# Optimization experiments

Hardware: AMD Instinct MI355X
Metric: run time of the kernel (lower is better)

Reference implementation:

```python
import jax, jax.numpy as jnp
import numpy as np

DIM = 512
NUM_HEADS = 8
HEAD_DIM = DIM // NUM_HEADS
SCALE = HEAD_DIM ** -0.5
B, N = 8, 1024


def setup_inputs() -> dict:
    key = jax.random.key(0)
    k1, k2, k3, k4, k5 = jax.random.split(key, 5)
    x = jax.random.normal(k1, (B, N, DIM), dtype=jnp.float32)
    rpe_bias = jax.random.normal(k2, (1, NUM_HEADS, N, N), dtype=jnp.float32)
    # torch Linear weights: [out_features, in_features], y = x @ W.T
    qkv_w = jax.random.normal(k3, (3 * DIM, DIM), dtype=jnp.float32) * (DIM ** -0.5)
    proj_w = jax.random.normal(k4, (DIM, DIM), dtype=jnp.float32) * (DIM ** -0.5)
    proj_b = jax.random.normal(k5, (DIM,), dtype=jnp.float32) * 0.01
    return {"x": x, "rpe_bias": rpe_bias, "qkv_w": qkv_w, "proj_w": proj_w, "proj_b": proj_b}


def reference(x, rpe_bias, qkv_w, proj_w, proj_b):
    b, n, c = x.shape
    h, d = NUM_HEADS, HEAD_DIM
    # qkv projection (no bias): [B,N,3C] -> [3,B,H,N,D]
    qkv = (x @ qkv_w.T).reshape(b, n, 3, h, d).transpose(2, 0, 3, 1, 4)
    q, k, v = qkv[0], qkv[1], qkv[2]
    attn = jnp.einsum('bhnd,bhmd->bhnm', q, k) * SCALE + rpe_bias
    attn = jax.nn.softmax(attn, axis=-1)  # dropout p=0 -> identity
    out = jnp.einsum('bhnm,bhmd->bhnd', attn, v)
    out = out.transpose(0, 2, 1, 3).reshape(b, n, c)
    return out @ proj_w.T + proj_b
```

## Files before the change

### kernel.cpp

```cpp
#include <hip/hip_runtime.h>
#include <hip/hip_bf16.h>

#define B_    8
#define N_    1024
#define DIM_  512
#define H_    8
#define DH_   64
#define SCALE_ 0.125f

typedef unsigned short u16;
typedef __attribute__((ext_vector_type(8))) short bf16x8;
typedef __attribute__((ext_vector_type(4))) float f32x4;

__device__ __forceinline__ u16 f2bf(float f) {
  union { float f; unsigned u; } v; v.f = f;
  return (u16)((v.u + 0x7fffu + ((v.u >> 16) & 1u)) >> 16);
}
__device__ __forceinline__ unsigned pack2(float a, float b) {
  return (unsigned)f2bf(a) | ((unsigned)f2bf(b) << 16);
}
__device__ __forceinline__ void cp16(const void* g, void* l) {
  __builtin_amdgcn_global_load_lds(
      (const __attribute__((address_space(1))) unsigned*)g,
      (__attribute__((address_space(3))) unsigned*)l, 16, 0, 0);
}

__global__ __launch_bounds__(256) void convert_kernel(
    const float* __restrict__ X, const float* __restrict__ Wq,
    const float* __restrict__ Wp, u16* __restrict__ Xb,
    u16* __restrict__ Wqb, u16* __restrict__ Wpb) {
  const int NX4 = (B_ * N_ * DIM_) / 4;
  const int NQ4 = (3 * DIM_ * DIM_) / 4;
  const int NP4 = (DIM_ * DIM_) / 4;
  const int total = NX4 + NQ4 + NP4;
  const int stride = gridDim.x * 256;
  for (int i = blockIdx.x * 256 + threadIdx.x; i < total; i += stride) {
    const float* s; u16* d; int off;
    if (i < NX4)            { s = X;  d = Xb;  off = i; }
    else if (i < NX4 + NQ4) { s = Wq; d = Wqb; off = i - NX4; }
    else                    { s = Wp; d = Wpb; off = i - NX4 - NQ4; }
    float4 f = *(const float4*)(s + (size_t)off * 4);
    uint2 u; u.x = pack2(f.x, f.y); u.y = pack2(f.z, f.w);
    *(uint2*)(d + (size_t)off * 4) = u;
  }
}

__global__ __launch_bounds__(256) void qkv_gemm(
    const u16* __restrict__ Ab, const u16* __restrict__ Bb,
    u16* __restrict__ Q, u16* __restrict__ K, u16* __restrict__ Vt) {
  __shared__ __align__(16) u16 sA[128 * 64];
  __shared__ __align__(16) u16 sB[128 * 64];
  const int t = threadIdx.x;
  const int wv = t >> 6, lane = t & 63, quad = (lane >> 4) & 3, l15 = lane & 15;
  const int wr = wv >> 1, wc = wv & 1;
  const int m0 = blockIdx.y * 128;
  const int n0 = blockIdx.x * 128;

  const int srow = lane >> 3;
  const int schunk = (lane & 7) ^ srow;
  const size_t ga = (size_t)(m0 + srow) * DIM_ + schunk * 8;
  const size_t gb = (size_t)(n0 + srow) * DIM_ + schunk * 8;

  f32x4 zero = {0.f, 0.f, 0.f, 0.f};
  f32x4 acc[4][4];
#pragma unroll
  for (int i = 0; i < 4; i++)
#pragma unroll
    for (int j = 0; j < 4; j++) acc[i][j] = zero;

  for (int k0 = 0; k0 < DIM_; k0 += 64) {
    __syncthreads();
#pragma unroll
    for (int i = 0; i < 4; i++) {
      const int rb = 32 * wv + 8 * i;
      cp16(Ab + ga + (size_t)rb * DIM_ + k0, &sA[rb * 64]);
      cp16(Bb + gb + (size_t)rb * DIM_ + k0, &sB[rb * 64]);
    }
    __syncthreads();
#pragma unroll
    for (int ks = 0; ks < 2; ks++) {
      bf16x8 af[4], bfv[4];
#pragma unroll
      for (int i = 0; i < 4; i++)
        af[i] = *(const bf16x8*)&sA[(wr * 64 + 16 * i + l15) * 64 +
                                    (((ks << 2) | quad) ^ (l15 & 7)) * 8];
#pragma unroll
      for (int j = 0; j < 4; j++)
        bfv[j] = *(const bf16x8*)&sB[(wc * 64 + 16 * j + l15) * 64 +
                                     (((ks << 2) | quad) ^ (l15 & 7)) * 8];
#pragma unroll
      for (int i = 0; i < 4; i++)
#pragma unroll
        for (int j = 0; j < 4; j++)
          acc[i][j] = __builtin_amdgcn_mfma_f32_16x16x32_bf16(af[i], bfv[j], acc[i][j], 0, 0, 0);
    }
  }

  const int tsel = n0 >> 9;
#pragma unroll
  for (int j = 0; j < 4; j++) {
    const int jg = n0 + wc * 64 + 16 * j + l15;
    const int h = (jg >> 6) & 7, d = jg & 63;
#pragma unroll
    for (int i = 0; i < 4; i++) {
      const int mbase = m0 + wr * 64 + 16 * i + quad * 4;
      const int b = mbase >> 10, nb = mbase & 1023;
      const size_t bh = (size_t)(b * H_ + h);
      if (tsel == 2) {
        ushort4 v4;
        v4.x = f2bf(acc[i][j][0]); v4.y = f2bf(acc[i][j][1]);
        v4.z = f2bf(acc[i][j][2]); v4.w = f2bf(acc[i][j][3]);
        *(ushort4*)&Vt[(bh * DH_ + d) * N_ + nb] = v4;
      } else {
        u16* dst = (tsel == 0 ? Q : K);
#pragma unroll
        for (int rr = 0; rr < 4; rr++)
          dst[(bh * N_ + nb + rr) * DH_ + d] = f2bf(acc[i][j][rr]);
      }
    }
  }
}

__global__ __launch_bounds__(256) void attn_kernel(
    const u16* __restrict__ Q, const u16* __restrict__ K,
    const u16* __restrict__ Vt, const float* __restrict__ bias,
    u16* __restrict__ AO) {
  __shared__ __align__(16) u16 sK[64 * 72];
  __shared__ __align__(16) u16 sV[64 * 72];
  __shared__ __align__(16) u16 sP[64 * 72];
  const int t = threadIdx.x;
  const int wv = t >> 6, lane = t & 63, quad = (lane >> 4) & 3, l15 = lane & 15;
  const int n0 = blockIdx.x * 64;
  const int bh = blockIdx.y;
  const int b = bh >> 3, h = bh & 7;
  const int r = t >> 2, c = (t & 3) << 4;

  const int qg = n0 + 16 * wv + l15;
  bf16x8 qf0, qf1;
  {
    const u16* qsrc = Q + (((size_t)bh << 10) + qg) * DH_ + (quad << 3);
    qf0 = *(const bf16x8*)qsrc;
    qf1 = *(const bf16x8*)(qsrc + 32);
  }

  const float* bp = bias + (((size_t)h << 10) + qg) * N_ + (quad << 2);
  const u16* kbase = K + (((size_t)bh << 10) + r) * DH_ + c;
  const u16* vbase = Vt + (((size_t)bh << 6) + r) * N_ + c;

  f32x4 zero = {0.f, 0.f, 0.f, 0.f};
  f32x4 O[4];
  O[0] = zero; O[1] = zero; O[2] = zero; O[3] = zero;
  float lsum = 0.f;

  uint4 ka = *(const uint4*)kbase, kb2 = *(const uint4*)(kbase + 8);
  uint4 va = *(const uint4*)vbase, vb2 = *(const uint4*)(vbase + 8);
  float4 bias4[4];
#pragma unroll
  for (int cb = 0; cb < 4; cb++) bias4[cb] = *(const float4*)(bp + 16 * cb);

  for (int kt = 0; kt < 16; kt++) {
    __syncthreads();
    *(uint4*)&sK[r * 72 + c] = ka;  *(uint4*)&sK[r * 72 + c + 8] = kb2;
    *(uint4*)&sV[r * 72 + c] = va;  *(uint4*)&sV[r * 72 + c + 8] = vb2;
    if (kt < 15) {
      const u16* kn = kbase + (size_t)(kt + 1) * 64 * DH_;
      const u16* vn = vbase + (kt + 1) * 64;
      ka = *(const uint4*)kn; kb2 = *(const uint4*)(kn + 8);
      va = *(const uint4*)vn; vb2 = *(const uint4*)(vn + 8);
    }
    __syncthreads();

    f32x4 S[4];
    S[0] = zero; S[1] = zero; S[2] = zero; S[3] = zero;
#pragma unroll
    for (int ks = 0; ks < 2; ks++) {
      const bf16x8 qf = ks ? qf1 : qf0;
#pragma unroll
      for (int cb = 0; cb < 4; cb++) {
        bf16x8 kf = *(const bf16x8*)&sK[(16 * cb + l15) * 72 + ks * 32 + (quad << 3)];
        S[cb] = __builtin_amdgcn_mfma_f32_16x16x32_bf16(kf, qf, S[cb], 0, 0, 0);
      }
    }

#pragma unroll
    for (int cb = 0; cb < 4; cb++) {
      float p0 = __expf(fmaf(S[cb][0], SCALE_, bias4[cb].x));
      float p1 = __expf(fmaf(S[cb][1], SCALE_, bias4[cb].y));
      float p2 = __expf(fmaf(S[cb][2], SCALE_, bias4[cb].z));
      float p3 = __expf(fmaf(S[cb][3], SCALE_, bias4[cb].w));
      lsum += (p0 + p1) + (p2 + p3);
      uint2 pk;
      pk.x = pack2(p0, p1);
      pk.y = pack2(p2, p3);
      *(uint2*)&sP[(16 * wv + l15) * 72 + 16 * cb + (quad << 2)] = pk;
    }
    if (kt < 15) {
      const float* bn = bp + (kt + 1) * 64;
#pragma unroll
      for (int cb = 0; cb < 4; cb++) bias4[cb] = *(const float4*)(bn + 16 * cb);
    }
    asm volatile("s_waitcnt lgkmcnt(0)" ::: "memory");

#pragma unroll
    for (int ks = 0; ks < 2; ks++) {
      bf16x8 pf = *(const bf16x8*)&sP[(16 * wv + l15) * 72 + ks * 32 + (quad << 3)];
#pragma unroll
      for (int cb = 0; cb < 4; cb++) {
        bf16x8 vf = *(const bf16x8*)&sV[(16 * cb + l15) * 72 + ks * 32 + (quad << 3)];
        O[cb] = __builtin_amdgcn_mfma_f32_16x16x32_bf16(vf, pf, O[cb], 0, 0, 0);
      }
    }
  }

  lsum += __shfl_xor(lsum, 16);
  lsum += __shfl_xor(lsum, 32);
  const float inv = 1.f / lsum;
#pragma unroll
  for (int cb = 0; cb < 4; cb++) {
    ushort4 o4;
    o4.x = f2bf(O[cb][0] * inv); o4.y = f2bf(O[cb][1] * inv);
    o4.z = f2bf(O[cb][2] * inv); o4.w = f2bf(O[cb][3] * inv);
    *(ushort4*)&AO[(((size_t)b << 10) + qg) * DIM_ + h * DH_ + 16 * cb + (quad << 2)] = o4;
  }
}

__global__ __launch_bounds__(256) void proj_gemm(
    const u16* __restrict__ Ab, const u16* __restrict__ Bb,
    const float* __restrict__ Pb, float* __restrict__ Out) {
  __shared__ __align__(16) u16 sA[128 * 64];
  __shared__ __align__(16) u16 sB[128 * 64];
  const int t = threadIdx.x;
  const int wv = t >> 6, lane = t & 63, quad = (lane >> 4) & 3, l15 = lane & 15;
  const int wr = wv >> 1, wc = wv & 1;
  const int m0 = blockIdx.y * 128;
  const int n0 = blockIdx.x * 128;

  const int srow = lane >> 3;
  const int schunk = (lane & 7) ^ srow;
  const size_t ga = (size_t)(m0 + srow) * DIM_ + schunk * 8;
  const size_t gb = (size_t)(n0 + srow) * DIM_ + schunk * 8;

  f32x4 zero = {0.f, 0.f, 0.f, 0.f};
  f32x4 acc[4][4];
#pragma unroll
  for (int i = 0; i < 4; i++)
#pragma unroll
    for (int j = 0; j < 4; j++) acc[i][j] = zero;

  for (int k0 = 0; k0 < DIM_; k0 += 64) {
    __syncthreads();
#pragma unroll
    for (int i = 0; i < 4; i++) {
      const int rb = 32 * wv + 8 * i;
      cp16(Ab + ga + (size_t)rb * DIM_ + k0, &sA[rb * 64]);
      cp16(Bb + gb + (size_t)rb * DIM_ + k0, &sB[rb * 64]);
    }
    __syncthreads();
#pragma unroll
    for (int ks = 0; ks < 2; ks++) {
      bf16x8 af[4], bfv[4];
#pragma unroll
      for (int i = 0; i < 4; i++)
        af[i] = *(const bf16x8*)&sA[(wr * 64 + 16 * i + l15) * 64 +
                                    (((ks << 2) | quad) ^ (l15 & 7)) * 8];
#pragma unroll
      for (int j = 0; j < 4; j++)
        bfv[j] = *(const bf16x8*)&sB[(wc * 64 + 16 * j + l15) * 64 +
                                     (((ks << 2) | quad) ^ (l15 & 7)) * 8];
#pragma unroll
      for (int i = 0; i < 4; i++)
#pragma unroll
        for (int j = 0; j < 4; j++)
          acc[i][j] = __builtin_amdgcn_mfma_f32_16x16x32_bf16(af[i], bfv[j], acc[i][j], 0, 0, 0);
    }
  }

#pragma unroll
  for (int j = 0; j < 4; j++) {
    const int jg = n0 + wc * 64 + 16 * j + l15;
    const float pb = Pb[jg];
#pragma unroll
    for (int i = 0; i < 4; i++) {
      const int mbase = m0 + wr * 64 + 16 * i + quad * 4;
#pragma unroll
      for (int rr = 0; rr < 4; rr++)
        Out[(size_t)(mbase + rr) * DIM_ + jg] = acc[i][j][rr] + pb;
    }
  }
}

extern "C" void kernel_launch(void* const* d_in, const int* in_sizes, int n_in,
                              void* d_out, int out_size, void* d_ws, size_t ws_size,
                              hipStream_t stream) {
  const float* x      = (const float*)d_in[0];
  const float* rpe    = (const float*)d_in[1];
  const float* qkv_w  = (const float*)d_in[2];
  const float* proj_w = (const float*)d_in[3];
  const float* proj_b = (const float*)d_in[4];
  float* out = (float*)d_out;

  const size_t perbuf = (size_t)B_ * N_ * DIM_;
  u16* Xb  = (u16*)d_ws;
  u16* Q   = Xb + perbuf;
  u16* K   = Q + perbuf;
  u16* Vt  = K + perbuf;
  u16* Wqb = Vt + perbuf;
  u16* Wpb = Wqb + (size_t)3 * DIM_ * DIM_;
  u16* AO  = Xb;

  convert_kernel<<<2560, 256, 0, stream>>>(x, qkv_w, proj_w, Xb, Wqb, Wpb);
  qkv_gemm<<<dim3(12, 64), 256, 0, stream>>>(Xb, Wqb, Q, K, Vt);
  attn_kernel<<<dim3(16, 64), 256, 0, stream>>>(Q, K, Vt, rpe, AO);
  proj_gemm<<<dim3(4, 64), 256, 0, stream>>>(AO, Wpb, proj_b, out);
}
```

Baseline: 176.6 us.

## Shrink GEMM tiles, keep P in registers, swizzle LDS, remap attention grid

The QKV and projection GEMMs switch from 128x128 to 128x64 tiles, doubling the block count and adding launch bounds for higher occupancy. The attention kernel drops the sP shared buffer and feeds P straight from registers into 16x16x16 MFMAs. It replaces padded K/V shared layouts with XOR-swizzled ones, adds s_setprio around the MFMA phases, and remaps blocks so neighbouring blocks share a head and reuse the bias in L2. Together these cut LDS traffic and barriers, in exchange for more V fragment loads and more MFMA instructions.

After: 173.7 us. Within noise of the previous version (-1.7%).

```diff
diff --git a/kernel.cpp b/kernel.cpp
--- a/kernel.cpp
+++ b/kernel.cpp
@@ -10,6 +10,7 @@
 
 typedef unsigned short u16;
 typedef __attribute__((ext_vector_type(8))) short bf16x8;
+typedef __attribute__((ext_vector_type(4))) short bf16x4;
 typedef __attribute__((ext_vector_type(4))) float f32x4;
 
 __device__ __forceinline__ u16 f2bf(float f) {
@@ -45,16 +46,15 @@
   }
 }
 
-__global__ __launch_bounds__(256) void qkv_gemm(
+__global__ __launch_bounds__(256, 4) void qkv_gemm(
     const u16* __restrict__ Ab, const u16* __restrict__ Bb,
     u16* __restrict__ Q, u16* __restrict__ K, u16* __restrict__ Vt) {
   __shared__ __align__(16) u16 sA[128 * 64];
-  __shared__ __align__(16) u16 sB[128 * 64];
+  __shared__ __align__(16) u16 sB[64 * 64];
   const int t = threadIdx.x;
   const int wv = t >> 6, lane = t & 63, quad = (lane >> 4) & 3, l15 = lane & 15;
-  const int wr = wv >> 1, wc = wv & 1;
   const int m0 = blockIdx.y * 128;
-  const int n0 = blockIdx.x * 128;
+  const int n0 = blockIdx.x * 64;
 
   const int srow = lane >> 3;
   const int schunk = (lane & 7) ^ srow;
@@ -62,9 +62,9 @@
   const size_t gb = (size_t)(n0 + srow) * DIM_ + schunk * 8;
 
   f32x4 zero = {0.f, 0.f, 0.f, 0.f};
-  f32x4 acc[4][4];
-#pragma unroll
-  for (int i = 0; i < 4; i++)
+  f32x4 acc[2][4];
+#pragma unroll
+  for (int i = 0; i < 2; i++)
 #pragma unroll
     for (int j = 0; j < 4; j++) acc[i][j] = zero;
 
@@ -74,22 +74,26 @@
     for (int i = 0; i < 4; i++) {
       const int rb = 32 * wv + 8 * i;
       cp16(Ab + ga + (size_t)rb * DIM_ + k0, &sA[rb * 64]);
+    }
+#pragma unroll
+    for (int i = 0; i < 2; i++) {
+      const int rb = 16 * wv + 8 * i;
       cp16(Bb + gb + (size_t)rb * DIM_ + k0, &sB[rb * 64]);
     }
     __syncthreads();
 #pragma unroll
     for (int ks = 0; ks < 2; ks++) {
-      bf16x8 af[4], bfv[4];
-#pragma unroll
-      for (int i = 0; i < 4; i++)
-        af[i] = *(const bf16x8*)&sA[(wr * 64 + 16 * i + l15) * 64 +
+      bf16x8 af[2], bfv[4];
+#pragma unroll
+      for (int i = 0; i < 2; i++)
+        af[i] = *(const bf16x8*)&sA[(wv * 32 + 16 * i + l15) * 64 +
                                     (((ks << 2) | quad) ^ (l15 & 7)) * 8];
 #pragma unroll
       for (int j = 0; j < 4; j++)
-        bfv[j] = *(const bf16x8*)&sB[(wc * 64 + 16 * j + l15) * 64 +
+        bfv[j] = *(const bf16x8*)&sB[(16 * j + l15) * 64 +
                                      (((ks << 2) | quad) ^ (l15 & 7)) * 8];
 #pragma unroll
-      for (int i = 0; i < 4; i++)
+      for (int i = 0; i < 2; i++)
 #pragma unroll
         for (int j = 0; j < 4; j++)
           acc[i][j] = __builtin_amdgcn_mfma_f32_16x16x32_bf16(af[i], bfv[j], acc[i][j], 0, 0, 0);
@@ -99,11 +103,11 @@
   const int tsel = n0 >> 9;
 #pragma unroll
   for (int j = 0; j < 4; j++) {
-    const int jg = n0 + wc * 64 + 16 * j + l15;
+    const int jg = n0 + 16 * j + l15;
     const int h = (jg >> 6) & 7, d = jg & 63;
 #pragma unroll
-    for (int i = 0; i < 4; i++) {
-      const int mbase = m0 + wr * 64 + 16 * i + quad * 4;
+    for (int i = 0; i < 2; i++) {
+      const int mbase = m0 + wv * 32 + 16 * i + quad * 4;
       const int b = mbase >> 10, nb = mbase & 1023;
       const size_t bh = (size_t)(b * H_ + h);
       if (tsel == 2) {
@@ -121,95 +125,111 @@
   }
 }
 
-__global__ __launch_bounds__(256) void attn_kernel(
+__global__ __launch_bounds__(256, 4) void attn_kernel(
     const u16* __restrict__ Q, const u16* __restrict__ K,
     const u16* __restrict__ Vt, const float* __restrict__ bias,
     u16* __restrict__ AO) {
-  __shared__ __align__(16) u16 sK[64 * 72];
-  __shared__ __align__(16) u16 sV[64 * 72];
-  __shared__ __align__(16) u16 sP[64 * 72];
+  __shared__ __align__(16) u16 sK[64 * 64];
+  __shared__ __align__(16) u16 sV[64 * 64];
   const int t = threadIdx.x;
   const int wv = t >> 6, lane = t & 63, quad = (lane >> 4) & 3, l15 = lane & 15;
-  const int n0 = blockIdx.x * 64;
-  const int bh = blockIdx.y;
-  const int b = bh >> 3, h = bh & 7;
+
+  const int bid = blockIdx.x;
+  const int h = bid & 7;
+  const int s = bid >> 3;
+  const int nx = s >> 3;
+  const int b = s & 7;
+  const int n0 = nx << 6;
+  const int bh = b * H_ + h;
   const int r = t >> 2, c = (t & 3) << 4;
 
   const int qg = n0 + 16 * wv + l15;
   bf16x8 qf0, qf1;
   {
-    const u16* qsrc = Q + (((size_t)bh << 10) + qg) * DH_ + (quad << 3);
-    qf0 = *(const bf16x8*)qsrc;
-    qf1 = *(const bf16x8*)(qsrc + 32);
+    const u16* qa = Q + (((size_t)bh << 10) + qg) * DH_ + (quad << 3);
+    qf0 = *(const bf16x8*)qa; qf1 = *(const bf16x8*)(qa + 32);
   }
 
   const float* bp = bias + (((size_t)h << 10) + qg) * N_ + (quad << 2);
   const u16* kbase = K + (((size_t)bh << 10) + r) * DH_ + c;
   const u16* vbase = Vt + (((size_t)bh << 6) + r) * N_ + c;
+
+  const int so0 = r * 128 + ((((t & 3) << 5)) ^ ((r & 7) << 4));
+  const int so1 = r * 128 + ((((t & 3) << 5) + 16) ^ ((r & 7) << 4));
+  const int rx = (l15 & 7) << 4;
+  const int frow = l15 * 128;
+  const int vhalf = (quad & 1) << 3;
 
   f32x4 zero = {0.f, 0.f, 0.f, 0.f};
   f32x4 O[4];
   O[0] = zero; O[1] = zero; O[2] = zero; O[3] = zero;
   float lsum = 0.f;
 
-  uint4 ka = *(const uint4*)kbase, kb2 = *(const uint4*)(kbase + 8);
-  uint4 va = *(const uint4*)vbase, vb2 = *(const uint4*)(vbase + 8);
-  float4 bias4[4];
-#pragma unroll
-  for (int cb = 0; cb < 4; cb++) bias4[cb] = *(const float4*)(bp + 16 * cb);
+  uint4 k0r = *(const uint4*)kbase, k1r = *(const uint4*)(kbase + 8);
+  uint4 v0r = *(const uint4*)vbase, v1r = *(const uint4*)(vbase + 8);
 
   for (int kt = 0; kt < 16; kt++) {
     __syncthreads();
-    *(uint4*)&sK[r * 72 + c] = ka;  *(uint4*)&sK[r * 72 + c + 8] = kb2;
-    *(uint4*)&sV[r * 72 + c] = va;  *(uint4*)&sV[r * 72 + c + 8] = vb2;
+    *(uint4*)((char*)sK + so0) = k0r; *(uint4*)((char*)sK + so1) = k1r;
+    *(uint4*)((char*)sV + so0) = v0r; *(uint4*)((char*)sV + so1) = v1r;
     if (kt < 15) {
       const u16* kn = kbase + (size_t)(kt + 1) * 64 * DH_;
       const u16* vn = vbase + (kt + 1) * 64;
-      ka = *(const uint4*)kn; kb2 = *(const uint4*)(kn + 8);
-      va = *(const uint4*)vn; vb2 = *(const uint4*)(vn + 8);
-    }
-    __syncthreads();
+      k0r = *(const uint4*)kn; k1r = *(const uint4*)(kn + 8);
+      v0r = *(const uint4*)vn; v1r = *(const uint4*)(vn + 8);
+    }
+    float4 b4[4];
+#pragma unroll
+    for (int cb = 0; cb < 4; cb++)
+      b4[cb] = *(const float4*)(bp + (kt << 6) + 16 * cb);
+    __syncthreads();
+
+    bf16x8 kf[8];
+#pragma unroll
+    for (int ks = 0; ks < 2; ks++)
+#pragma unroll
+      for (int cb = 0; cb < 4; cb++)
+        kf[ks * 4 + cb] = *(const bf16x8*)((const char*)sK + cb * 2048 + frow +
+                                           (((ks << 6) | (quad << 4)) ^ rx));
 
     f32x4 S[4];
     S[0] = zero; S[1] = zero; S[2] = zero; S[3] = zero;
+    __builtin_amdgcn_s_setprio(1);
 #pragma unroll
     for (int ks = 0; ks < 2; ks++) {
       const bf16x8 qf = ks ? qf1 : qf0;
 #pragma unroll
+      for (int cb = 0; cb < 4; cb++)
+        S[cb] = __builtin_amdgcn_mfma_f32_16x16x32_bf16(kf[ks * 4 + cb], qf, S[cb], 0, 0, 0);
+    }
+    __builtin_amdgcn_s_setprio(0);
+
+    bf16x4 p[4];
+#pragma unroll
+    for (int cb = 0; cb < 4; cb++) {
+      float p0 = __expf(fmaf(S[cb][0], SCALE_, b4[cb].x));
+      float p1 = __expf(fmaf(S[cb][1], SCALE_, b4[cb].y));
+      float p2 = __expf(fmaf(S[cb][2], SCALE_, b4[cb].z));
+      float p3 = __expf(fmaf(S[cb][3], SCALE_, b4[cb].w));
+      lsum += (p0 + p1) + (p2 + p3);
+      uint2 pk; pk.x = pack2(p0, p1); pk.y = pack2(p2, p3);
+      p[cb] = __builtin_bit_cast(bf16x4, pk);
+    }
+
+    __builtin_amdgcn_s_setprio(1);
+#pragma unroll
+    for (int cbp = 0; cbp < 4; cbp++) {
+      bf16x4 vf[4];
+#pragma unroll
       for (int cb = 0; cb < 4; cb++) {
-        bf16x8 kf = *(const bf16x8*)&sK[(16 * cb + l15) * 72 + ks * 32 + (quad << 3)];
-        S[cb] = __builtin_amdgcn_mfma_f32_16x16x32_bf16(kf, qf, S[cb], 0, 0, 0);
+        const int ch = ((((2 * cb + (quad >> 1)) << 4)) ^ rx) + vhalf;
+        vf[cb] = *(const bf16x4*)((const char*)sV + cbp * 2048 + frow + ch);
       }
-    }
-
-#pragma unroll
-    for (int cb = 0; cb < 4; cb++) {
-      float p0 = __expf(fmaf(S[cb][0], SCALE_, bias4[cb].x));
-      float p1 = __expf(fmaf(S[cb][1], SCALE_, bias4[cb].y));
-      float p2 = __expf(fmaf(S[cb][2], SCALE_, bias4[cb].z));
-      float p3 = __expf(fmaf(S[cb][3], SCALE_, bias4[cb].w));
-      lsum += (p0 + p1) + (p2 + p3);
-      uint2 pk;
-      pk.x = pack2(p0, p1);
-      pk.y = pack2(p2, p3);
-      *(uint2*)&sP[(16 * wv + l15) * 72 + 16 * cb + (quad << 2)] = pk;
-    }
-    if (kt < 15) {
-      const float* bn = bp + (kt + 1) * 64;
-#pragma unroll
-      for (int cb = 0; cb < 4; cb++) bias4[cb] = *(const float4*)(bn + 16 * cb);
-    }
-    asm volatile("s_waitcnt lgkmcnt(0)" ::: "memory");
-
-#pragma unroll
-    for (int ks = 0; ks < 2; ks++) {
-      bf16x8 pf = *(const bf16x8*)&sP[(16 * wv + l15) * 72 + ks * 32 + (quad << 3)];
-#pragma unroll
-      for (int cb = 0; cb < 4; cb++) {
-        bf16x8 vf = *(const bf16x8*)&sV[(16 * cb + l15) * 72 + ks * 32 + (quad << 3)];
-        O[cb] = __builtin_amdgcn_mfma_f32_16x16x32_bf16(vf, pf, O[cb], 0, 0, 0);
-      }
-    }
+#pragma unroll
+      for (int cb = 0; cb < 4; cb++)
+        O[cbp] = __builtin_amdgcn_mfma_f32_16x16x16bf16_1k(vf[cb], p[cb], O[cbp], 0, 0, 0);
+    }
+    __builtin_amdgcn_s_setprio(0);
   }
 
   lsum += __shfl_xor(lsum, 16);
@@ -220,20 +240,20 @@
     ushort4 o4;
     o4.x = f2bf(O[cb][0] * inv); o4.y = f2bf(O[cb][1] * inv);
     o4.z = f2bf(O[cb][2] * inv); o4.w = f2bf(O[cb][3] * inv);
-    *(ushort4*)&AO[(((size_t)b << 10) + qg) * DIM_ + h * DH_ + 16 * cb + (quad << 2)] = o4;
-  }
-}
-
-__global__ __launch_bounds__(256) void proj_gemm(
+    *(ushort4*)&AO[(((size_t)bh << 10 | (size_t)0) * 0) +
+                   (((size_t)b << 10) + qg) * DIM_ + h * DH_ + 16 * cb + (quad << 2)] = o4;
+  }
+}
+
+__global__ __launch_bounds__(256, 4) void proj_gemm(
     const u16* __restrict__ Ab, const u16* __restrict__ Bb,
     const float* __restrict__ Pb, float* __restrict__ Out) {
   __shared__ __align__(16) u16 sA[128 * 64];
-  __shared__ __align__(16) u16 sB[128 * 64];
+  __shared__ __align__(16) u16 sB[64 * 64];
   const int t = threadIdx.x;
   const int wv = t >> 6, lane = t & 63, quad = (lane >> 4) & 3, l15 = lane & 15;
-  const int wr = wv >> 1, wc = wv & 1;
   const int m0 = blockIdx.y * 128;
-  const int n0 = blockIdx.x * 128;
+  const int n0 = blockIdx.x * 64;
 
   const int srow = lane >> 3;
   const int schunk = (lane & 7) ^ srow;
@@ -241,9 +261,9 @@
   const size_t gb = (size_t)(n0 + srow) * DIM_ + schunk * 8;
 
   f32x4 zero = {0.f, 0.f, 0.f, 0.f};
-  f32x4 acc[4][4];
-#pragma unroll
-  for (int i = 0; i < 4; i++)
+  f32x4 acc[2][4];
+#pragma unroll
+  for (int i = 0; i < 2; i++)
 #pragma unroll
     for (int j = 0; j < 4; j++) acc[i][j] = zero;
 
@@ -253,22 +273,26 @@
     for (int i = 0; i < 4; i++) {
       const int rb = 32 * wv + 8 * i;
       cp16(Ab + ga + (size_t)rb * DIM_ + k0, &sA[rb * 64]);
+    }
+#pragma unroll
+    for (int i = 0; i < 2; i++) {
+      const int rb = 16 * wv + 8 * i;
       cp16(Bb + gb + (size_t)rb * DIM_ + k0, &sB[rb * 64]);
     }
     __syncthreads();
 #pragma unroll
     for (int ks = 0; ks < 2; ks++) {
-      bf16x8 af[4], bfv[4];
-#pragma unroll
-      for (int i = 0; i < 4; i++)
-        af[i] = *(const bf16x8*)&sA[(wr * 64 + 16 * i + l15) * 64 +
+      bf16x8 af[2], bfv[4];
+#pragma unroll
+      for (int i = 0; i < 2; i++)
+        af[i] = *(const bf16x8*)&sA[(wv * 32 + 16 * i + l15) * 64 +
                                     (((ks << 2) | quad) ^ (l15 & 7)) * 8];
 #pragma unroll
       for (int j = 0; j < 4; j++)
-        bfv[j] = *(const bf16x8*)&sB[(wc * 64 + 16 * j + l15) * 64 +
+        bfv[j] = *(const bf16x8*)&sB[(16 * j + l15) * 64 +
                                      (((ks << 2) | quad) ^ (l15 & 7)) * 8];
 #pragma unroll
-      for (int i = 0; i < 4; i++)
+      for (int i = 0; i < 2; i++)
 #pragma unroll
         for (int j = 0; j < 4; j++)
           acc[i][j] = __builtin_amdgcn_mfma_f32_16x16x32_bf16(af[i], bfv[j], acc[i][j], 0, 0, 0);
@@ -277,11 +301,11 @@
 
 #pragma unroll
   for (int j = 0; j < 4; j++) {
-    const int jg = n0 + wc * 64 + 16 * j + l15;
+    const int jg = n0 + 16 * j + l15;
     const float pb = Pb[jg];
 #pragma unroll
-    for (int i = 0; i < 4; i++) {
-      const int mbase = m0 + wr * 64 + 16 * i + quad * 4;
+    for (int i = 0; i < 2; i++) {
+      const int mbase = m0 + wv * 32 + 16 * i + quad * 4;
 #pragma unroll
       for (int rr = 0; rr < 4; rr++)
         Out[(size_t)(mbase + rr) * DIM_ + jg] = acc[i][j][rr] + pb;
@@ -309,7 +333,7 @@
   u16* AO  = Xb;
 
   convert_kernel<<<2560, 256, 0, stream>>>(x, qkv_w, proj_w, Xb, Wqb, Wpb);
-  qkv_gemm<<<dim3(12, 64), 256, 0, stream>>>(Xb, Wqb, Q, K, Vt);
-  attn_kernel<<<dim3(16, 64), 256, 0, stream>>>(Q, K, Vt, rpe, AO);
-  proj_gemm<<<dim3(4, 64), 256, 0, stream>>>(AO, Wpb, proj_b, out);
-}
+  qkv_gemm<<<dim3(24, 64), 256, 0, stream>>>(Xb, Wqb, Q, K, Vt);
+  attn_kernel<<<1024, 256, 0, stream>>>(Q, K, Vt, rpe, AO);
+  proj_gemm<<<dim3(8, 64), 256, 0, stream>>>(AO, Wpb, proj_b, out);
+}
```
